# Kernel tuning notes

Hardware: AMD Instinct MI355X
Metric: run time of the kernel (lower is better)

The kernel has to match this reference:

```python
import jax, jax.numpy as jnp
import numpy as np

EPS_LN = 1e-5
EPS_D = 1e-8
K = 3

def layer_norm(x, g, b):
    mu = jnp.mean(x, axis=-1, keepdims=True)
    var = jnp.var(x, axis=-1, keepdims=True)
    return (x - mu) * jax.lax.rsqrt(var + EPS_LN) * g + b

def setup_inputs() -> dict:
    key = jax.random.key(0)
    ks = jax.random.split(key, 8)
    Nc, Nu, Cin, Cout = 4096, 16384, 256, 256
    return {
        "x_feat": jax.random.normal(ks[0], (Nc, Cin), jnp.float32),
        "x_pos": jax.random.uniform(ks[1], (Nc, 3), jnp.float32),
        "xup_feat": jax.random.normal(ks[2], (Nu, Cout), jnp.float32),
        "xup_pos": jax.random.uniform(ks[3], (Nu, 3), jnp.float32),
        "g1": jnp.ones((Cin,), jnp.float32),
        "b1": jnp.zeros((Cin,), jnp.float32),
        "W": jax.random.normal(ks[4], (Cin, Cout), jnp.float32) * 0.02,
        "b": jnp.zeros((Cout,), jnp.float32),
        "g2": jnp.ones((Cout,), jnp.float32),
        "b2": jnp.zeros((Cout,), jnp.float32),
        "W_up": jax.random.normal(ks[5], (Cout, Cout), jnp.float32) * 0.02,
        "b_up": jnp.zeros((Cout,), jnp.float32),
    }

def reference(x_feat, x_pos, xup_feat, xup_pos, g1, b1, W, b, g2, b2, W_up, b_up):
    # norm -> linear on coarse points: [Nc, Cout]
    x = layer_norm(x_feat, g1, b1) @ W + b
    # norm -> linear on fine points:   [Nu, Cout]
    xu = layer_norm(xup_feat, g2, b2) @ W_up + b_up
    # squared pairwise distances fine->coarse: [Nu, Nc]
    d2 = (jnp.sum(xup_pos * xup_pos, axis=-1, keepdims=True)
          - 2.0 * (xup_pos @ x_pos.T)
          + jnp.sum(x_pos * x_pos, axis=-1))
    # k nearest coarse neighbors per fine point
    neg_d2, idx = jax.lax.top_k(-d2, K)          # [Nu, K]
    w = 1.0 / (-neg_d2 + EPS_D)                  # inverse-distance weights
    w = w / jnp.sum(w, axis=-1, keepdims=True)
    # gather + weighted sum: [Nu, Cout]
    interp = jnp.einsum('uk,ukc->uc', w, x[idx])
    return interp + xu
```

## Files before the change

### kernel.cpp

```cpp
#include <hip/hip_runtime.h>

#define EPS_LN 1e-5f
#define EPS_D  1e-8f

typedef __attribute__((ext_vector_type(8))) short s16x8;
typedef __attribute__((ext_vector_type(4))) float f32x4;

#define XC_OFF   0u
#define MU_OFF   4194304u
#define RS_OFF   4276224u
#define CP_OFF   4358144u
#define WTH_OFF  4423680u
#define WTL_OFF  4554752u
#define WUTH_OFF 4685824u
#define WUTL_OFF 4816896u

__global__ __launch_bounds__(256) void prep_kernel(
    const float* __restrict__ x_feat, const float* __restrict__ xup_feat,
    const float* __restrict__ x_pos,
    const float* __restrict__ W, const float* __restrict__ W_up,
    float* __restrict__ mu, float* __restrict__ rs, float4* __restrict__ cp,
    unsigned short* __restrict__ wth, unsigned short* __restrict__ wtl,
    unsigned short* __restrict__ wuth, unsigned short* __restrict__ wutl)
{
    const int bid = blockIdx.x, tid = threadIdx.x;
    const int lane = tid & 63, wave = tid >> 6;

    if (bid < 320) {
        for (int r = bid * 4 + wave; r < 20480; r += 1280) {
            const float* src = (r < 16384) ? (xup_feat + (size_t)r * 256)
                                           : (x_feat + (size_t)(r - 16384) * 256);
            const float4 v = ((const float4*)src)[lane];
            float s  = v.x + v.y + v.z + v.w;
            float ss = v.x*v.x + v.y*v.y + v.z*v.z + v.w*v.w;
            #pragma unroll
            for (int off = 1; off < 64; off <<= 1) {
                s  += __shfl_xor(s,  off);
                ss += __shfl_xor(ss, off);
            }
            if (lane == 0) {
                const float m   = s * (1.0f / 256.0f);
                const float var = ss * (1.0f / 256.0f) - m * m;
                mu[r] = m;
                rs[r] = rsqrtf(var + EPS_LN);
            }
        }
    } else if (bid < 336) {
        const int mb = bid - 320;
        const float* src = (mb < 8) ? W : W_up;
        unsigned short* dh = (mb < 8) ? wth : wuth;
        unsigned short* dl = (mb < 8) ? wtl : wutl;
        const int k  = (mb & 7) * 32 + (tid >> 3);
        const int n0 = (tid & 7) * 32;
        for (int i = 0; i < 32; i += 4) {
            const float4 v = *(const float4*)&src[(size_t)k * 256 + n0 + i];
            const float vv[4] = { v.x, v.y, v.z, v.w };
            #pragma unroll
            for (int c = 0; c < 4; ++c) {
                const unsigned ua = __float_as_uint(vv[c]);
                const unsigned hb = ua & 0xFFFF0000u;
                const float rr = vv[c] - __uint_as_float(hb);
                const size_t o = (size_t)(n0 + i + c) * 256 + k;
                dh[o] = (unsigned short)(ua >> 16);
                dl[o] = (unsigned short)(__float_as_uint(rr) >> 16);
            }
        }
    } else {
        const int i = (bid - 336) * 256 + tid;
        if (i < 4096) {
            const float px = x_pos[i * 3 + 0];
            const float py = x_pos[i * 3 + 1];
            const float pz = x_pos[i * 3 + 2];
            cp[i] = make_float4(px, py, pz, px * px + py * py + pz * pz);
        }
    }
}

__global__ __launch_bounds__(256) void gemm_kernel(
    const float* __restrict__ Xf, const float* __restrict__ Xc,
    const float* __restrict__ mu, const float* __restrict__ rs,
    const float* __restrict__ g2, const float* __restrict__ b2,
    const float* __restrict__ g1, const float* __restrict__ b1,
    const unsigned short* __restrict__ wuth, const unsigned short* __restrict__ wutl,
    const unsigned short* __restrict__ wth,  const unsigned short* __restrict__ wtl,
    const float* __restrict__ b_up, const float* __restrict__ bb,
    float* __restrict__ outF, float* __restrict__ outC)
{
    const int bid = blockIdx.x;
    const float *X, *gg, *bt, *bias; const unsigned short *BH, *BL; float* OUT;
    int row0, col0, statoff;
    if (bid < 256) {
        X = Xf; gg = g2; bt = b2; BH = wuth; BL = wutl; bias = b_up; OUT = outF;
        row0 = (bid >> 1) * 128; col0 = (bid & 1) * 128; statoff = 0;
    } else {
        const int id = bid - 256;
        X = Xc; gg = g1; bt = b1; BH = wth; BL = wtl; bias = bb; OUT = outC;
        row0 = (id >> 1) * 128; col0 = (id & 1) * 128; statoff = 16384;
    }

    const int lane = threadIdx.x & 63;
    const int wave = threadIdx.x >> 6;
    const int wr = wave >> 1, wc = wave & 1;
    const int lm = lane & 15, lk = lane >> 4;

    int arow[4]; float amu[4], ars[4];
    #pragma unroll
    for (int mf = 0; mf < 4; ++mf) {
        arow[mf] = row0 + wr * 64 + mf * 16 + lm;
        amu[mf] = mu[statoff + arow[mf]];
        ars[mf] = rs[statoff + arow[mf]];
    }
    int ncol[4]; float bv[4];
    #pragma unroll
    for (int nf = 0; nf < 4; ++nf) {
        ncol[nf] = col0 + wc * 64 + nf * 16 + lm;
        bv[nf] = bias[ncol[nf]];
    }

    f32x4 acc[4][4];
    #pragma unroll
    for (int mf = 0; mf < 4; ++mf)
        #pragma unroll
        for (int nf = 0; nf < 4; ++nf)
            acc[mf][nf] = (f32x4){0.0f, 0.0f, 0.0f, 0.0f};

    for (int k0 = 0; k0 < 256; k0 += 32) {
        const int kb = k0 + lk * 8;
        const float4 gq0 = *(const float4*)(gg + kb);
        const float4 gq1 = *(const float4*)(gg + kb + 4);
        const float4 bq0 = *(const float4*)(bt + kb);
        const float4 bq1 = *(const float4*)(bt + kb + 4);
        const float gv[8] = { gq0.x, gq0.y, gq0.z, gq0.w, gq1.x, gq1.y, gq1.z, gq1.w };
        const float bw[8] = { bq0.x, bq0.y, bq0.z, bq0.w, bq1.x, bq1.y, bq1.z, bq1.w };

        s16x8 ah[4], al[4];
        #pragma unroll
        for (int mf = 0; mf < 4; ++mf) {
            const float* pa = X + (size_t)arow[mf] * 256 + kb;
            const float4 x0 = *(const float4*)pa;
            const float4 x1 = *(const float4*)(pa + 4);
            const float xs[8] = { x0.x, x0.y, x0.z, x0.w, x1.x, x1.y, x1.z, x1.w };
            #pragma unroll
            for (int j = 0; j < 8; ++j) {
                const float sj = ars[mf] * gv[j];
                const float tj = fmaf(-amu[mf], sj, bw[j]);
                const float a  = fmaf(xs[j], sj, tj);
                const unsigned ua = __float_as_uint(a);
                const unsigned hb = ua & 0xFFFF0000u;
                const float rr = a - __uint_as_float(hb);
                ah[mf][j] = (short)(ua >> 16);
                al[mf][j] = (short)(__float_as_uint(rr) >> 16);
            }
        }
        s16x8 bh[4], bl[4];
        #pragma unroll
        for (int nf = 0; nf < 4; ++nf) {
            const size_t o = (size_t)ncol[nf] * 256 + kb;
            bh[nf] = *(const s16x8*)(BH + o);
            bl[nf] = *(const s16x8*)(BL + o);
        }
        #pragma unroll
        for (int mf = 0; mf < 4; ++mf)
            #pragma unroll
            for (int nf = 0; nf < 4; ++nf) {
                acc[mf][nf] = __builtin_amdgcn_mfma_f32_16x16x32_bf16(ah[mf], bh[nf], acc[mf][nf], 0, 0, 0);
                acc[mf][nf] = __builtin_amdgcn_mfma_f32_16x16x32_bf16(ah[mf], bl[nf], acc[mf][nf], 0, 0, 0);
                acc[mf][nf] = __builtin_amdgcn_mfma_f32_16x16x32_bf16(al[mf], bh[nf], acc[mf][nf], 0, 0, 0);
            }
    }

    #pragma unroll
    for (int mf = 0; mf < 4; ++mf) {
        #pragma unroll
        for (int q = 0; q < 4; ++q) {
            const size_t ro = (size_t)(row0 + wr * 64 + mf * 16 + lk * 4 + q) * 256;
            #pragma unroll
            for (int nf = 0; nf < 4; ++nf)
                OUT[ro + ncol[nf]] = acc[mf][nf][q] + bv[nf];
        }
    }
}

__global__ __launch_bounds__(512) void topk_kernel(
    const float4* __restrict__ cp, const float* __restrict__ xup_pos,
    const float* __restrict__ xc, float* __restrict__ out)
{
    __shared__ float pd[8][64][3];
    __shared__ int   pi[8][64][3];
    __shared__ float wsel[64][3];
    __shared__ int   isel[64][3];

    const int tid = threadIdx.x, lane = tid & 63, wave = tid >> 6;
    const int u = blockIdx.x * 64 + lane;

    const float ux = xup_pos[u * 3 + 0];
    const float uy = xup_pos[u * 3 + 1];
    const float uz = xup_pos[u * 3 + 2];
    const float uu = ux * ux + uy * uy + uz * uz;

    float b0 = 3.402823466e+38f, b1 = b0, b2 = b0;
    int i0 = 0, i1 = 0, i2 = 0;

    const int j0 = wave * 512;
    #pragma unroll 4
    for (int j = j0; j < j0 + 512; ++j) {
        const float4 c = cp[j];
        const float dot = ux * c.x + uy * c.y + uz * c.z;
        const float d = (uu - 2.0f * dot) + c.w;
        const bool lt0 = d < b0, lt1 = d < b1, lt2 = d < b2;
        const float n1 = lt0 ? b0 : (lt1 ? d : b1);
        const int  ni1 = lt0 ? i0 : (lt1 ? j : i1);
        const float n2 = lt1 ? b1 : (lt2 ? d : b2);
        const int  ni2 = lt1 ? i1 : (lt2 ? j : i2);
        b0 = lt0 ? d : b0;  i0 = lt0 ? j : i0;
        b1 = n1; i1 = ni1;
        b2 = n2; i2 = ni2;
    }

    pd[wave][lane][0] = b0; pd[wave][lane][1] = b1; pd[wave][lane][2] = b2;
    pi[wave][lane][0] = i0; pi[wave][lane][1] = i1; pi[wave][lane][2] = i2;
    __syncthreads();

    if (wave == 0) {
        for (int w = 1; w < 8; ++w) {
            #pragma unroll
            for (int e = 0; e < 3; ++e) {
                const float d = pd[w][lane][e];
                const int  ci = pi[w][lane][e];
                const bool lt0 = (d < b0) || (d == b0 && ci < i0);
                const bool lt1 = (d < b1) || (d == b1 && ci < i1);
                const bool lt2 = (d < b2) || (d == b2 && ci < i2);
                const float n1 = lt0 ? b0 : (lt1 ? d : b1);
                const int  ni1 = lt0 ? i0 : (lt1 ? ci : i1);
                const float n2 = lt1 ? b1 : (lt2 ? d : b2);
                const int  ni2 = lt1 ? i1 : (lt2 ? ci : i2);
                b0 = lt0 ? d : b0;  i0 = lt0 ? ci : i0;
                b1 = n1; i1 = ni1;
                b2 = n2; i2 = ni2;
            }
        }
        float w0 = 1.0f / (b0 + EPS_D);
        float w1 = 1.0f / (b1 + EPS_D);
        float w2 = 1.0f / (b2 + EPS_D);
        const float inv = 1.0f / (w0 + w1 + w2);
        wsel[lane][0] = w0 * inv; wsel[lane][1] = w1 * inv; wsel[lane][2] = w2 * inv;
        isel[lane][0] = i0; isel[lane][1] = i1; isel[lane][2] = i2;
    }
    __syncthreads();

    #pragma unroll
    for (int r = 0; r < 8; ++r) {
        const int ul = wave * 8 + r;
        const float w0 = wsel[ul][0], w1 = wsel[ul][1], w2 = wsel[ul][2];
        const int a0 = isel[ul][0], a1 = isel[ul][1], a2 = isel[ul][2];
        const float4 v0 = ((const float4*)(xc + (size_t)a0 * 256))[lane];
        const float4 v1 = ((const float4*)(xc + (size_t)a1 * 256))[lane];
        const float4 v2 = ((const float4*)(xc + (size_t)a2 * 256))[lane];
        float4* op = (float4*)(out + (size_t)(blockIdx.x * 64 + ul) * 256);
        float4 o = op[lane];
        o.x += w0 * v0.x + w1 * v1.x + w2 * v2.x;
        o.y += w0 * v0.y + w1 * v1.y + w2 * v2.y;
        o.z += w0 * v0.z + w1 * v1.z + w2 * v2.z;
        o.w += w0 * v0.w + w1 * v1.w + w2 * v2.w;
        op[lane] = o;
    }
}

extern "C" void kernel_launch(void* const* d_in, const int* in_sizes, int n_in,
                              void* d_out, int out_size, void* d_ws, size_t ws_size,
                              hipStream_t stream)
{
    const float* x_feat   = (const float*)d_in[0];
    const float* x_pos    = (const float*)d_in[1];
    const float* xup_feat = (const float*)d_in[2];
    const float* xup_pos  = (const float*)d_in[3];
    const float* g1       = (const float*)d_in[4];
    const float* b1       = (const float*)d_in[5];
    const float* W        = (const float*)d_in[6];
    const float* bb       = (const float*)d_in[7];
    const float* g2       = (const float*)d_in[8];
    const float* b2       = (const float*)d_in[9];
    const float* W_up     = (const float*)d_in[10];
    const float* b_up     = (const float*)d_in[11];

    float* out = (float*)d_out;
    char*  ws  = (char*)d_ws;

    float* xc  = (float*)(ws + XC_OFF);
    float* mu  = (float*)(ws + MU_OFF);
    float* rs  = (float*)(ws + RS_OFF);
    float4* cp = (float4*)(ws + CP_OFF);
    unsigned short* wth  = (unsigned short*)(ws + WTH_OFF);
    unsigned short* wtl  = (unsigned short*)(ws + WTL_OFF);
    unsigned short* wuth = (unsigned short*)(ws + WUTH_OFF);
    unsigned short* wutl = (unsigned short*)(ws + WUTL_OFF);

    prep_kernel<<<352, 256, 0, stream>>>(x_feat, xup_feat, x_pos, W, W_up,
                                         mu, rs, cp, wth, wtl, wuth, wutl);
    gemm_kernel<<<320, 256, 0, stream>>>(xup_feat, x_feat, mu, rs,
                                         g2, b2, g1, b1,
                                         wuth, wutl, wth, wtl,
                                         b_up, bb, out, xc);
    topk_kernel<<<256, 512, 0, stream>>>(cp, xup_pos, xc, out);
}
```

Baseline: 202.2 us.

## Replace brute-force kNN scan with uniform 8x8x8 spatial grid search

Adds a single-block kernel that bins coarse points into an 8x8x8 uniform grid using counting sort, storing sorted positions, original indices and cell start offsets. The top-k kernel now scans only the 27 neighbouring cells, split across waves, instead of all 4096 coarse points. If the third-best distance exceeds the guaranteed search radius, it falls back to a full scan on wave 0. The GEMM inner loop is also reordered so A fragments are built and consumed per row fragment, which lowers register pressure. Costs include an extra serial single-block launch, a possibly divergent fallback, and tie-breaking among equal distances that no longer follows the original index order.

After: 173.8 us. -14.0%, faster.

```diff
diff --git a/kernel.cpp b/kernel.cpp
--- a/kernel.cpp
+++ b/kernel.cpp
@@ -6,20 +6,21 @@
 typedef __attribute__((ext_vector_type(8))) short s16x8;
 typedef __attribute__((ext_vector_type(4))) float f32x4;
 
-#define XC_OFF   0u
-#define MU_OFF   4194304u
-#define RS_OFF   4276224u
-#define CP_OFF   4358144u
-#define WTH_OFF  4423680u
-#define WTL_OFF  4554752u
-#define WUTH_OFF 4685824u
-#define WUTL_OFF 4816896u
+#define XC_OFF     0u
+#define MU_OFF     4194304u
+#define RS_OFF     4276224u
+#define WTH_OFF    4358144u
+#define WTL_OFF    4489216u
+#define WUTH_OFF   4620288u
+#define WUTL_OFF   4751360u
+#define CPS_OFF    4882432u
+#define IDXS_OFF   4947968u
+#define CST_OFF    4964352u
 
 __global__ __launch_bounds__(256) void prep_kernel(
     const float* __restrict__ x_feat, const float* __restrict__ xup_feat,
-    const float* __restrict__ x_pos,
     const float* __restrict__ W, const float* __restrict__ W_up,
-    float* __restrict__ mu, float* __restrict__ rs, float4* __restrict__ cp,
+    float* __restrict__ mu, float* __restrict__ rs,
     unsigned short* __restrict__ wth, unsigned short* __restrict__ wtl,
     unsigned short* __restrict__ wuth, unsigned short* __restrict__ wutl)
 {
@@ -45,7 +46,7 @@
                 rs[r] = rsqrtf(var + EPS_LN);
             }
         }
-    } else if (bid < 336) {
+    } else {
         const int mb = bid - 320;
         const float* src = (mb < 8) ? W : W_up;
         unsigned short* dh = (mb < 8) ? wth : wuth;
@@ -65,14 +66,65 @@
                 dl[o] = (unsigned short)(__float_as_uint(rr) >> 16);
             }
         }
-    } else {
-        const int i = (bid - 336) * 256 + tid;
-        if (i < 4096) {
-            const float px = x_pos[i * 3 + 0];
-            const float py = x_pos[i * 3 + 1];
-            const float pz = x_pos[i * 3 + 2];
-            cp[i] = make_float4(px, py, pz, px * px + py * py + pz * pz);
-        }
+    }
+}
+
+__device__ __forceinline__ int cell_of(float px, float py, float pz) {
+    int cx = (int)(px * 8.0f); cx = cx < 0 ? 0 : (cx > 7 ? 7 : cx);
+    int cy = (int)(py * 8.0f); cy = cy < 0 ? 0 : (cy > 7 ? 7 : cy);
+    int cz = (int)(pz * 8.0f); cz = cz < 0 ? 0 : (cz > 7 ? 7 : cz);
+    return (cz * 8 + cy) * 8 + cx;
+}
+
+__global__ __launch_bounds__(1024) void grid_kernel(
+    const float* __restrict__ x_pos,
+    float4* __restrict__ cps, int* __restrict__ idxs, int* __restrict__ cellStart)
+{
+    __shared__ int cnt[512];
+    __shared__ int ofs[512];
+    __shared__ int wsum[8];
+
+    const int tid = threadIdx.x, lane = tid & 63;
+    if (tid < 512) cnt[tid] = 0;
+    __syncthreads();
+
+    for (int i = tid; i < 4096; i += 1024) {
+        const int c = cell_of(x_pos[i*3+0], x_pos[i*3+1], x_pos[i*3+2]);
+        atomicAdd(&cnt[c], 1);
+    }
+    __syncthreads();
+
+    int v = 0, incl = 0;
+    if (tid < 512) {
+        v = cnt[tid];
+        incl = v;
+        #pragma unroll
+        for (int off = 1; off < 64; off <<= 1) {
+            const int t = __shfl_up(incl, off);
+            if (lane >= off) incl += t;
+        }
+        if (lane == 63) wsum[tid >> 6] = incl;
+    }
+    __syncthreads();
+    if (tid == 0) {
+        int run = 0;
+        for (int w = 0; w < 8; ++w) { const int t = wsum[w]; wsum[w] = run; run += t; }
+    }
+    __syncthreads();
+    if (tid < 512) {
+        const int excl = incl - v + wsum[tid >> 6];
+        ofs[tid] = excl;
+        cellStart[tid] = excl;
+    }
+    if (tid == 0) cellStart[512] = 4096;
+    __syncthreads();
+
+    for (int i = tid; i < 4096; i += 1024) {
+        const float px = x_pos[i*3+0], py = x_pos[i*3+1], pz = x_pos[i*3+2];
+        const int c = cell_of(px, py, pz);
+        const int p = atomicAdd(&ofs[c], 1);
+        cps[p] = make_float4(px, py, pz, px*px + py*py + pz*pz);
+        idxs[p] = i;
     }
 }
 
@@ -126,6 +178,15 @@
 
     for (int k0 = 0; k0 < 256; k0 += 32) {
         const int kb = k0 + lk * 8;
+
+        s16x8 bh[4], bl[4];
+        #pragma unroll
+        for (int nf = 0; nf < 4; ++nf) {
+            const size_t o = (size_t)ncol[nf] * 256 + kb;
+            bh[nf] = *(const s16x8*)(BH + o);
+            bl[nf] = *(const s16x8*)(BL + o);
+        }
+
         const float4 gq0 = *(const float4*)(gg + kb);
         const float4 gq1 = *(const float4*)(gg + kb + 4);
         const float4 bq0 = *(const float4*)(bt + kb);
@@ -133,13 +194,13 @@
         const float gv[8] = { gq0.x, gq0.y, gq0.z, gq0.w, gq1.x, gq1.y, gq1.z, gq1.w };
         const float bw[8] = { bq0.x, bq0.y, bq0.z, bq0.w, bq1.x, bq1.y, bq1.z, bq1.w };
 
-        s16x8 ah[4], al[4];
         #pragma unroll
         for (int mf = 0; mf < 4; ++mf) {
             const float* pa = X + (size_t)arow[mf] * 256 + kb;
             const float4 x0 = *(const float4*)pa;
             const float4 x1 = *(const float4*)(pa + 4);
             const float xs[8] = { x0.x, x0.y, x0.z, x0.w, x1.x, x1.y, x1.z, x1.w };
+            s16x8 ah, al;
             #pragma unroll
             for (int j = 0; j < 8; ++j) {
                 const float sj = ars[mf] * gv[j];
@@ -148,25 +209,16 @@
                 const unsigned ua = __float_as_uint(a);
                 const unsigned hb = ua & 0xFFFF0000u;
                 const float rr = a - __uint_as_float(hb);
-                ah[mf][j] = (short)(ua >> 16);
-                al[mf][j] = (short)(__float_as_uint(rr) >> 16);
-            }
-        }
-        s16x8 bh[4], bl[4];
-        #pragma unroll
-        for (int nf = 0; nf < 4; ++nf) {
-            const size_t o = (size_t)ncol[nf] * 256 + kb;
-            bh[nf] = *(const s16x8*)(BH + o);
-            bl[nf] = *(const s16x8*)(BL + o);
-        }
-        #pragma unroll
-        for (int mf = 0; mf < 4; ++mf)
+                ah[j] = (short)(ua >> 16);
+                al[j] = (short)(__float_as_uint(rr) >> 16);
+            }
             #pragma unroll
             for (int nf = 0; nf < 4; ++nf) {
-                acc[mf][nf] = __builtin_amdgcn_mfma_f32_16x16x32_bf16(ah[mf], bh[nf], acc[mf][nf], 0, 0, 0);
-                acc[mf][nf] = __builtin_amdgcn_mfma_f32_16x16x32_bf16(ah[mf], bl[nf], acc[mf][nf], 0, 0, 0);
-                acc[mf][nf] = __builtin_amdgcn_mfma_f32_16x16x32_bf16(al[mf], bh[nf], acc[mf][nf], 0, 0, 0);
-            }
+                acc[mf][nf] = __builtin_amdgcn_mfma_f32_16x16x32_bf16(ah, bh[nf], acc[mf][nf], 0, 0, 0);
+                acc[mf][nf] = __builtin_amdgcn_mfma_f32_16x16x32_bf16(ah, bl[nf], acc[mf][nf], 0, 0, 0);
+                acc[mf][nf] = __builtin_amdgcn_mfma_f32_16x16x32_bf16(al, bh[nf], acc[mf][nf], 0, 0, 0);
+            }
+        }
     }
 
     #pragma unroll
@@ -181,70 +233,105 @@
     }
 }
 
+#define BIGD 3.402823466e+38f
+
+__device__ __forceinline__ void ins3(float d, int p,
+    float& b0, float& b1, float& b2, int& p0, int& p1, int& p2)
+{
+    const bool lt0 = d < b0, lt1 = d < b1, lt2 = d < b2;
+    const float n1 = lt0 ? b0 : (lt1 ? d : b1);
+    const int   q1 = lt0 ? p0 : (lt1 ? p : p1);
+    const float n2 = lt1 ? b1 : (lt2 ? d : b2);
+    const int   q2 = lt1 ? p1 : (lt2 ? p : p2);
+    b0 = lt0 ? d : b0;  p0 = lt0 ? p : p0;
+    b1 = n1; p1 = q1;
+    b2 = n2; p2 = q2;
+}
+
 __global__ __launch_bounds__(512) void topk_kernel(
-    const float4* __restrict__ cp, const float* __restrict__ xup_pos,
+    const float4* __restrict__ cps, const int* __restrict__ idxs,
+    const int* __restrict__ cellStart,
+    const float* __restrict__ xup_pos,
     const float* __restrict__ xc, float* __restrict__ out)
 {
     __shared__ float pd[8][64][3];
-    __shared__ int   pi[8][64][3];
+    __shared__ int   pp[8][64][3];
     __shared__ float wsel[64][3];
     __shared__ int   isel[64][3];
+    __shared__ int   cst[513];
 
     const int tid = threadIdx.x, lane = tid & 63, wave = tid >> 6;
     const int u = blockIdx.x * 64 + lane;
+
+    for (int i = tid; i < 513; i += 512) cst[i] = cellStart[i];
 
     const float ux = xup_pos[u * 3 + 0];
     const float uy = xup_pos[u * 3 + 1];
     const float uz = xup_pos[u * 3 + 2];
     const float uu = ux * ux + uy * uy + uz * uz;
-
-    float b0 = 3.402823466e+38f, b1 = b0, b2 = b0;
-    int i0 = 0, i1 = 0, i2 = 0;
-
-    const int j0 = wave * 512;
-    #pragma unroll 4
-    for (int j = j0; j < j0 + 512; ++j) {
-        const float4 c = cp[j];
-        const float dot = ux * c.x + uy * c.y + uz * c.z;
-        const float d = (uu - 2.0f * dot) + c.w;
-        const bool lt0 = d < b0, lt1 = d < b1, lt2 = d < b2;
-        const float n1 = lt0 ? b0 : (lt1 ? d : b1);
-        const int  ni1 = lt0 ? i0 : (lt1 ? j : i1);
-        const float n2 = lt1 ? b1 : (lt2 ? d : b2);
-        const int  ni2 = lt1 ? i1 : (lt2 ? j : i2);
-        b0 = lt0 ? d : b0;  i0 = lt0 ? j : i0;
-        b1 = n1; i1 = ni1;
-        b2 = n2; i2 = ni2;
+    int cx = (int)(ux * 8.0f); cx = cx < 0 ? 0 : (cx > 7 ? 7 : cx);
+    int cy = (int)(uy * 8.0f); cy = cy < 0 ? 0 : (cy > 7 ? 7 : cy);
+    int cz = (int)(uz * 8.0f); cz = cz < 0 ? 0 : (cz > 7 ? 7 : cz);
+
+    __syncthreads();
+
+    float b0 = BIGD, b1 = BIGD, b2 = BIGD;
+    int p0 = 0, p1 = 0, p2 = 0;
+
+    for (int cc = wave; cc < 27; cc += 8) {
+        const int nx = cx + (cc % 3) - 1;
+        const int ny = cy + ((cc / 3) % 3) - 1;
+        const int nz = cz + (cc / 9) - 1;
+        if ((unsigned)nx > 7u || (unsigned)ny > 7u || (unsigned)nz > 7u) continue;
+        const int cell = (nz * 8 + ny) * 8 + nx;
+        const int s = cst[cell], e = cst[cell + 1];
+        if (s >= e) continue;
+        float4 c = cps[s];
+        for (int p = s; p < e; ++p) {
+            const float4 nxt = (p + 1 < e) ? cps[p + 1] : c;
+            const float dot = ux * c.x + uy * c.y + uz * c.z;
+            const float d = (uu - 2.0f * dot) + c.w;
+            ins3(d, p, b0, b1, b2, p0, p1, p2);
+            c = nxt;
+        }
     }
 
     pd[wave][lane][0] = b0; pd[wave][lane][1] = b1; pd[wave][lane][2] = b2;
-    pi[wave][lane][0] = i0; pi[wave][lane][1] = i1; pi[wave][lane][2] = i2;
+    pp[wave][lane][0] = p0; pp[wave][lane][1] = p1; pp[wave][lane][2] = p2;
     __syncthreads();
 
     if (wave == 0) {
         for (int w = 1; w < 8; ++w) {
             #pragma unroll
-            for (int e = 0; e < 3; ++e) {
-                const float d = pd[w][lane][e];
-                const int  ci = pi[w][lane][e];
-                const bool lt0 = (d < b0) || (d == b0 && ci < i0);
-                const bool lt1 = (d < b1) || (d == b1 && ci < i1);
-                const bool lt2 = (d < b2) || (d == b2 && ci < i2);
-                const float n1 = lt0 ? b0 : (lt1 ? d : b1);
-                const int  ni1 = lt0 ? i0 : (lt1 ? ci : i1);
-                const float n2 = lt1 ? b1 : (lt2 ? d : b2);
-                const int  ni2 = lt1 ? i1 : (lt2 ? ci : i2);
-                b0 = lt0 ? d : b0;  i0 = lt0 ? ci : i0;
-                b1 = n1; i1 = ni1;
-                b2 = n2; i2 = ni2;
-            }
-        }
+            for (int e = 0; e < 3; ++e)
+                ins3(pd[w][lane][e], pp[w][lane][e], b0, b1, b2, p0, p1, p2);
+        }
+
+        const float h = 0.125f;
+        float gmin = BIGD;
+        if (cx > 0) gmin = fminf(gmin, ux - (float)(cx - 1) * h);
+        if (cx < 7) gmin = fminf(gmin, (float)(cx + 2) * h - ux);
+        if (cy > 0) gmin = fminf(gmin, uy - (float)(cy - 1) * h);
+        if (cy < 7) gmin = fminf(gmin, (float)(cy + 2) * h - uy);
+        if (cz > 0) gmin = fminf(gmin, uz - (float)(cz - 1) * h);
+        if (cz < 7) gmin = fminf(gmin, (float)(cz + 2) * h - uz);
+
+        if (b2 > gmin * gmin) {
+            b0 = b1 = b2 = BIGD; p0 = p1 = p2 = 0;
+            for (int p = 0; p < 4096; ++p) {
+                const float4 c = cps[p];
+                const float dot = ux * c.x + uy * c.y + uz * c.z;
+                const float d = (uu - 2.0f * dot) + c.w;
+                ins3(d, p, b0, b1, b2, p0, p1, p2);
+            }
+        }
+
         float w0 = 1.0f / (b0 + EPS_D);
         float w1 = 1.0f / (b1 + EPS_D);
         float w2 = 1.0f / (b2 + EPS_D);
         const float inv = 1.0f / (w0 + w1 + w2);
         wsel[lane][0] = w0 * inv; wsel[lane][1] = w1 * inv; wsel[lane][2] = w2 * inv;
-        isel[lane][0] = i0; isel[lane][1] = i1; isel[lane][2] = i2;
+        isel[lane][0] = idxs[p0]; isel[lane][1] = idxs[p1]; isel[lane][2] = idxs[p2];
     }
     __syncthreads();
 
@@ -289,17 +376,20 @@
     float* xc  = (float*)(ws + XC_OFF);
     float* mu  = (float*)(ws + MU_OFF);
     float* rs  = (float*)(ws + RS_OFF);
-    float4* cp = (float4*)(ws + CP_OFF);
     unsigned short* wth  = (unsigned short*)(ws + WTH_OFF);
     unsigned short* wtl  = (unsigned short*)(ws + WTL_OFF);
     unsigned short* wuth = (unsigned short*)(ws + WUTH_OFF);
     unsigned short* wutl = (unsigned short*)(ws + WUTL_OFF);
-
-    prep_kernel<<<352, 256, 0, stream>>>(x_feat, xup_feat, x_pos, W, W_up,
-                                         mu, rs, cp, wth, wtl, wuth, wutl);
+    float4* cps = (float4*)(ws + CPS_OFF);
+    int* idxs   = (int*)(ws + IDXS_OFF);
+    int* cstart = (int*)(ws + CST_OFF);
+
+    prep_kernel<<<336, 256, 0, stream>>>(x_feat, xup_feat, W, W_up,
+                                         mu, rs, wth, wtl, wuth, wutl);
+    grid_kernel<<<1, 1024, 0, stream>>>(x_pos, cps, idxs, cstart);
     gemm_kernel<<<320, 256, 0, stream>>>(xup_feat, x_feat, mu, rs,
                                          g2, b2, g1, b1,
                                          wuth, wutl, wth, wtl,
                                          b_up, bb, out, xc);
-    topk_kernel<<<256, 512, 0, stream>>>(cp, xup_pos, xc, out);
-}
+    topk_kernel<<<256, 512, 0, stream>>>(cps, idxs, cstart, xup_pos, xc, out);
+}
```
